# Kernel tuning notes

Measured on AMD Instinct MI355X. Metric: run time of the kernel, lower is better.

The kernel has to match this reference:

```python
import jax, jax.numpy as jnp
import numpy as np

L = 2048
LEVEL = 4
B = 16
D = 32

# pywt 'db4' decomposition filters (dec_lo, dec_hi), hardcoded to avoid pywt dep
DB4_DEC_LO = np.array([
    -0.010597401784997278, 0.032883011666982945, 0.030841381835986965,
    -0.18703481171888114, -0.02798376941698385, 0.6308807679295904,
    0.7148465705525415, 0.23037781330885523])
DB4_DEC_HI = np.array([
    -0.23037781330885523, 0.7148465705525415, -0.6308807679295904,
    -0.02798376941698385, 0.18703481171888114, 0.030841381835986965,
    -0.032883011666982945, -0.010597401784997278])


def _wavelet_dec_filter(vec, length, level):
    # filter[j][t][(t - 2^j * i) mod L] = vec[i]  (vectorized over t, i)
    wl = len(vec)
    f = np.zeros((level, length, length), dtype=np.float32)
    t = np.arange(length)[:, None]
    i = np.arange(wl)[None, :]
    rows = np.broadcast_to(t, (length, wl))
    for j in range(level):
        idx = (t - (2 ** j) * i) % length  # (L, wl)
        f[j, rows, idx] = vec[None, :]
    return f


def setup_inputs() -> dict:
    key = jax.random.key(0)
    x = jax.random.normal(key, (B, L, D), dtype=jnp.float32)
    h = DB4_DEC_HI / np.sqrt(2.0)
    g = DB4_DEC_LO / np.sqrt(2.0)
    w_dec_filter = jnp.asarray(_wavelet_dec_filter(h, L, LEVEL))  # (J, L, L)
    v_dec_filter = jnp.asarray(_wavelet_dec_filter(g, L, LEVEL))  # (J, L, L)
    return {"x": x, "w_dec_filter": w_dec_filter, "v_dec_filter": v_dec_filter}


def reference(x, w_dec_filter, v_dec_filter):
    # MODWT: x (B, L, D) -> wavecoeff (B, D, L, level+1)
    xt = jnp.transpose(x, (0, 2, 1))  # (B, D, L)
    level = w_dec_filter.shape[0]
    v_j = xt
    vs = []
    for j in range(level):  # sequential over small fixed number of levels
        v_j = jnp.einsum('ml,bdl->bdm', v_dec_filter[j], v_j)
        vs.append(v_j)
    v = jnp.stack(vs, axis=2)  # (B, D, J, L)
    # inputs to each detail filter: [x, v_0, ..., v_{J-2}]
    v_prime = jnp.concatenate([xt[:, :, None, :], v[:, :, :-1, :]], axis=2)  # (B, D, J, L)
    w = jnp.einsum('jml,bdjl->bdjm', w_dec_filter, v_prime)  # (B, D, J, L)
    wavecoeff = jnp.concatenate([w, v[:, :, -1:, :]], axis=2)  # (B, D, J+1, L)
    return jnp.transpose(wavecoeff, (0, 1, 3, 2))  # (B, D, L, J+1)
```

## Files before the change

kernel.cpp:

```cpp
#include <hip/hip_runtime.h>

#define L_LEN 2048
#define N_D   32
#define DSPL  16
#define BLOCK 256
#define TILE  128
#define HALO  105
#define ROWS  (TILE + HALO)
#define LSTR  ROWS
#define LPAD  64
#define BUFSZ (DSPL * LSTR + LPAD)

constexpr float G_[8] = {
    (float)(-0.010597401784997278 / 1.4142135623730951),
    (float)( 0.032883011666982945 / 1.4142135623730951),
    (float)( 0.030841381835986965 / 1.4142135623730951),
    (float)(-0.18703481171888114  / 1.4142135623730951),
    (float)(-0.02798376941698385  / 1.4142135623730951),
    (float)( 0.6308807679295904   / 1.4142135623730951),
    (float)( 0.7148465705525415   / 1.4142135623730951),
    (float)( 0.23037781330885523  / 1.4142135623730951)};
constexpr float H_[8] = {
    (float)(-0.23037781330885523  / 1.4142135623730951),
    (float)( 0.7148465705525415   / 1.4142135623730951),
    (float)(-0.6308807679295904   / 1.4142135623730951),
    (float)(-0.02798376941698385  / 1.4142135623730951),
    (float)( 0.18703481171888114  / 1.4142135623730951),
    (float)( 0.030841381835986965 / 1.4142135623730951),
    (float)(-0.032883011666982945 / 1.4142135623730951),
    (float)(-0.010597401784997278 / 1.4142135623730951)};

template <int R, int PMIN, int LOG2D, int TPD, int CH, bool VLDS, bool VOUT>
__device__ __forceinline__ void level_pass(const float* __restrict__ src,
                                           float* __restrict__ dst,
                                           float* __restrict__ ob, int t) {
    constexpr int D = 1 << LOG2D;
    for (int u = t; u < DSPL * TPD; u += BLOCK) {
        const int d   = u / TPD;
        const int j   = u - d * TPD;
        const int off = j & (D - 1);
        const int blk = j >> LOG2D;
        const int p0  = PMIN + blk * (4 * D) + off;

        const float* s = src + d * LSTR + (p0 - 7 * D);
        float smp[11];
#pragma unroll
        for (int k = 0; k < 11; ++k) smp[k] = s[k * D];

        float* db = dst + d * LSTR;
        float* og = ob + (size_t)d * (L_LEN * 5);
#pragma unroll
        for (int r = 0; r < 4; ++r) {
            const int p = p0 + r * D;
            float w = 0.f, v = 0.f;
#pragma unroll
            for (int i = 0; i < 8; ++i) {
                w = fmaf(H_[i], smp[7 + r - i], w);
                v = fmaf(G_[i], smp[7 + r - i], v);
            }
            const bool valid = (p < ROWS);
            if (VLDS && valid) db[p] = v;
            if (valid && p >= HALO) {
                float* o = og + (size_t)(p - HALO) * 5;
                o[CH] = w;
                if (VOUT) o[4] = v;
            }
        }
    }
}

__global__ __launch_bounds__(BLOCK) void swt_db4_kernel(const float* __restrict__ x,
                                                        float* __restrict__ out) {
    __shared__ float bufA[BUFSZ];
    __shared__ float bufB[BUFSZ];

    const int t    = threadIdx.x;
    const int bid  = blockIdx.x;
    const int dg   = bid & 1;
    const int tile = (bid >> 1) & 15;
    const int b    = bid >> 5;
    const int m0   = tile * TILE;

    const float* xb = x + (size_t)b * (L_LEN * N_D) + dg * DSPL;
    float* ob = out + (((size_t)b * N_D + dg * DSPL) * L_LEN + m0) * 5;

    for (int idx = t; idx < DSPL * ROWS; idx += BLOCK) {
        const int p  = idx >> 4;
        const int d  = idx & 15;
        const int gm = (m0 + p - HALO) & (L_LEN - 1);
        bufA[d * LSTR + p] = xb[(size_t)gm * N_D + d];
    }
    __syncthreads();

    level_pass<226,   7, 0, 57, 0, true,  false>(bufA, bufB, ob, t);
    __syncthreads();
    level_pass<212,  21, 1, 54, 1, true,  false>(bufB, bufA, ob, t);
    __syncthreads();
    level_pass<184,  49, 2, 48, 2, true,  false>(bufA, bufB, ob, t);
    __syncthreads();
    level_pass<128, 105, 3, 32, 3, false, true >(bufB, bufA, ob, t);
}

extern "C" void kernel_launch(void* const* d_in, const int* in_sizes, int n_in,
                              void* d_out, int out_size, void* d_ws, size_t ws_size,
                              hipStream_t stream) {
    const float* x = (const float*)d_in[0];
    float* out = (float*)d_out;

    swt_db4_kernel<<<16 * 16 * 2, BLOCK, 0, stream>>>(x, out);
}
```

Baseline: 144.5 us.

## Stage detail coefficients in LDS and vectorize level passes with float4

Each thread now computes four consecutive outputs per level from float4 LDS loads instead of strided samples. The input load uses float4 global reads. Detail coefficients for the first three levels are staged in a shared buffer, and the last level writes all five channels per output point together, replacing scattered strided global stores spread across four passes. The cost is more shared memory, a wider sample window per thread, and some redundant halo computation.

```diff
diff --git a/kernel.cpp b/kernel.cpp
--- a/kernel.cpp
+++ b/kernel.cpp
@@ -6,10 +6,11 @@
 #define BLOCK 256
 #define TILE  128
 #define HALO  105
-#define ROWS  (TILE + HALO)
-#define LSTR  ROWS
-#define LPAD  64
-#define BUFSZ (DSPL * LSTR + LPAD)
+#define FPAD  8
+#define LSTR  236
+#define SLAB  (FPAD + DSPL * LSTR)
+#define WCH   132
+#define WSTR  (3 * WCH)
 
 constexpr float G_[8] = {
     (float)(-0.010597401784997278 / 1.4142135623730951),
@@ -30,49 +31,46 @@
     (float)(-0.032883011666982945 / 1.4142135623730951),
     (float)(-0.010597401784997278 / 1.4142135623730951)};
 
-template <int R, int PMIN, int LOG2D, int TPD, int CH, bool VLDS, bool VOUT>
-__device__ __forceinline__ void level_pass(const float* __restrict__ src,
-                                           float* __restrict__ dst,
-                                           float* __restrict__ ob, int t) {
-    constexpr int D = 1 << LOG2D;
+template <int NSMP, int PMIN, int D, int TPD, int CH>
+__device__ __forceinline__ void qlevel(const float* __restrict__ src,
+                                       float* __restrict__ dst,
+                                       float* __restrict__ wbuf, int t) {
     for (int u = t; u < DSPL * TPD; u += BLOCK) {
-        const int d   = u / TPD;
-        const int j   = u - d * TPD;
-        const int off = j & (D - 1);
-        const int blk = j >> LOG2D;
-        const int p0  = PMIN + blk * (4 * D) + off;
+        const int d  = u / TPD;
+        const int j  = u - d * TPD;
+        const int p0 = PMIN + 4 * j;
 
-        const float* s = src + d * LSTR + (p0 - 7 * D);
-        float smp[11];
+        const float* s = src + FPAD + d * LSTR + (p0 - (NSMP - 4));
+        float smp[NSMP];
 #pragma unroll
-        for (int k = 0; k < 11; ++k) smp[k] = s[k * D];
+        for (int q = 0; q < NSMP / 4; ++q) {
+            const float4 x4 = *(const float4*)(s + 4 * q);
+            smp[4 * q + 0] = x4.x; smp[4 * q + 1] = x4.y;
+            smp[4 * q + 2] = x4.z; smp[4 * q + 3] = x4.w;
+        }
 
-        float* db = dst + d * LSTR;
-        float* og = ob + (size_t)d * (L_LEN * 5);
+        float w[4], v[4];
 #pragma unroll
         for (int r = 0; r < 4; ++r) {
-            const int p = p0 + r * D;
-            float w = 0.f, v = 0.f;
+            w[r] = 0.f; v[r] = 0.f;
 #pragma unroll
             for (int i = 0; i < 8; ++i) {
-                w = fmaf(H_[i], smp[7 + r - i], w);
-                v = fmaf(G_[i], smp[7 + r - i], v);
-            }
-            const bool valid = (p < ROWS);
-            if (VLDS && valid) db[p] = v;
-            if (valid && p >= HALO) {
-                float* o = og + (size_t)(p - HALO) * 5;
-                o[CH] = w;
-                if (VOUT) o[4] = v;
+                const float sv = smp[(NSMP - 4) + r - D * i];
+                w[r] = fmaf(H_[i], sv, w[r]);
+                v[r] = fmaf(G_[i], sv, v[r]);
             }
         }
+        *(float4*)(dst + FPAD + d * LSTR + p0) = make_float4(v[0], v[1], v[2], v[3]);
+        if (p0 >= HALO - 1)
+            *(float4*)(wbuf + d * WSTR + CH * WCH + (p0 - (HALO - 1))) =
+                make_float4(w[0], w[1], w[2], w[3]);
     }
 }
 
 __global__ __launch_bounds__(BLOCK) void swt_db4_kernel(const float* __restrict__ x,
                                                         float* __restrict__ out) {
-    __shared__ float bufA[BUFSZ];
-    __shared__ float bufB[BUFSZ];
+    __shared__ float vb[2 * SLAB];
+    __shared__ float wb[DSPL * WSTR];
 
     const int t    = threadIdx.x;
     const int bid  = blockIdx.x;
@@ -84,21 +82,46 @@
     const float* xb = x + (size_t)b * (L_LEN * N_D) + dg * DSPL;
     float* ob = out + (((size_t)b * N_D + dg * DSPL) * L_LEN + m0) * 5;
 
-    for (int idx = t; idx < DSPL * ROWS; idx += BLOCK) {
-        const int p  = idx >> 4;
-        const int d  = idx & 15;
+    for (int idx = t; idx < LSTR * 4; idx += BLOCK) {
+        const int p  = idx >> 2;
+        const int dq = idx & 3;
         const int gm = (m0 + p - HALO) & (L_LEN - 1);
-        bufA[d * LSTR + p] = xb[(size_t)gm * N_D + d];
+        const float4 xv = *(const float4*)(xb + (size_t)gm * N_D + 4 * dq);
+        float* vp = vb + FPAD + p;
+        vp[(4 * dq + 0) * LSTR] = xv.x;
+        vp[(4 * dq + 1) * LSTR] = xv.y;
+        vp[(4 * dq + 2) * LSTR] = xv.z;
+        vp[(4 * dq + 3) * LSTR] = xv.w;
     }
     __syncthreads();
 
-    level_pass<226,   7, 0, 57, 0, true,  false>(bufA, bufB, ob, t);
+    qlevel<12,  4, 1, 58, 0>(vb,        vb + SLAB, wb, t);
     __syncthreads();
-    level_pass<212,  21, 1, 54, 1, true,  false>(bufB, bufA, ob, t);
+    qlevel<20, 20, 2, 54, 1>(vb + SLAB, vb,        wb, t);
     __syncthreads();
-    level_pass<184,  49, 2, 48, 2, true,  false>(bufA, bufB, ob, t);
+    qlevel<32, 48, 4, 47, 2>(vb,        vb + SLAB, wb, t);
     __syncthreads();
-    level_pass<128, 105, 3, 32, 3, false, true >(bufB, bufA, ob, t);
+
+    for (int idx = t; idx < DSPL * TILE; idx += BLOCK) {
+        const int d  = idx >> 7;
+        const int mm = idx & (TILE - 1);
+        const int p  = HALO + mm;
+        const float* s = vb + SLAB + FPAD + d * LSTR + p;
+        float w = 0.f, v = 0.f;
+#pragma unroll
+        for (int i = 0; i < 8; ++i) {
+            const float sv = s[-8 * i];
+            w = fmaf(H_[i], sv, w);
+            v = fmaf(G_[i], sv, v);
+        }
+        float* o = ob + ((size_t)d * L_LEN + mm) * 5;
+        const float* wsrc = wb + d * WSTR + 1 + mm;
+        o[0] = wsrc[0];
+        o[1] = wsrc[WCH];
+        o[2] = wsrc[2 * WCH];
+        o[3] = w;
+        o[4] = v;
+    }
 }
 
 extern "C" void kernel_launch(void* const* d_in, const int* in_sizes, int n_in,
```

After: 135.2 us, median of 2. -6.5%, faster.
